# Optimization experiments

Hardware: AMD Instinct MI355X
Metric: run time of the kernel (lower is better)

The kernel has to match this reference:

```python
import jax, jax.numpy as jnp
import numpy as np

BIT = 8      # shared-exponent mantissa bits (bf_conf.*_bit)
GSZ = 36     # block size (bf_conf.*_sz)


def bfp_quantize(x, bit=BIT, sz=GSZ):
    """Block floating point: groups of `sz` consecutive elements share one
    exponent e = floor(log2(max|x|)); each element keeps `bit` mantissa bits."""
    shape = x.shape
    flat = x.reshape(-1)
    n = flat.shape[0]
    pad = (-n) % sz
    flat = jnp.pad(flat, (0, pad))
    g = flat.reshape(-1, sz)                                   # [G, sz]
    maxabs = jnp.max(jnp.abs(g), axis=1, keepdims=True)
    e = jnp.floor(jnp.log2(jnp.where(maxabs > 0, maxabs, 1.0)))
    scale = jnp.exp2(e - (bit - 1))                            # lsb of shared-exp format
    q = jnp.round(g / scale) * scale
    q = jnp.where(maxabs > 0, q, 0.0)
    return q.reshape(-1)[:n].reshape(shape)


def setup_inputs() -> dict:
    key = jax.random.key(0)
    k1, k2, k3 = jax.random.split(key, 3)
    B, Cin, Cout, H, W, K = 16, 32, 32, 224, 224, 3
    x = jax.random.normal(k1, (B, Cin, H, W), dtype=jnp.float32)
    fan_in = Cin * K * K
    bound = 1.0 / np.sqrt(fan_in)
    weight = jax.random.uniform(k2, (Cout, Cin, K, K), jnp.float32, -bound, bound)
    bias = jax.random.uniform(k3, (Cout,), jnp.float32, -bound, bound)
    return {"x": x, "weight": weight, "bias": bias}


def reference(x, weight, bias):
    xq = bfp_quantize(x)          # f_i
    wq = bfp_quantize(weight)     # f_w
    out = jax.lax.conv_general_dilated(
        xq, wq,
        window_strides=(1, 1),
        padding=((1, 1), (1, 1)),
        rhs_dilation=(1, 1),
        feature_group_count=1,
        dimension_numbers=("NCHW", "OIHW", "NCHW"),
    )
    out = out + bias[None, :, None, None]
    out = bfp_quantize(out)       # f_o
    return out
```

## Files before the change

### kernel.cpp

```cpp
#include <hip/hip_runtime.h>
#include <hip/hip_bf16.h>

#define GSZ 36
static const int NX  = 16 * 32 * 224 * 224;
static const int NX4 = NX / 4;
static const int NW  = 32 * 32 * 3 * 3;
static const int GXN = (NX + GSZ - 1) / GSZ;
static const int HWp = 224 * 224;

typedef short bf16x8 __attribute__((ext_vector_type(8)));
typedef float f32x4  __attribute__((ext_vector_type(4)));

__device__ __forceinline__ unsigned div36(unsigned n) {
    return (unsigned)(((unsigned long long)n * 954437177ull) >> 35);
}
__device__ __forceinline__ float scale_from_max(float m) {
    int e = (int)((__float_as_uint(m) >> 23) & 0xffu) - 127;
    return __uint_as_float((unsigned)(e + 120) << 23);
}
__device__ __forceinline__ float inv_from_scale(float s) {
    return __uint_as_float(0x7F000000u - __float_as_uint(s));
}
__device__ __forceinline__ unsigned short f2bf(float f) {
    return (unsigned short)(__float_as_uint(f) >> 16);
}

__global__ void k_quant_wt(const float* __restrict__ w, unsigned short* __restrict__ wt) {
    int g = threadIdx.x;
    int base = g * GSZ;
    float v[GSZ];
    const float4* p = reinterpret_cast<const float4*>(w + base);
    #pragma unroll
    for (int i = 0; i < 9; ++i) {
        float4 t = p[i];
        v[4*i+0] = t.x; v[4*i+1] = t.y; v[4*i+2] = t.z; v[4*i+3] = t.w;
    }
    float m = 0.0f;
    #pragma unroll
    for (int i = 0; i < GSZ; ++i) m = fmaxf(m, fabsf(v[i]));
    if (m > 0.0f) {
        float s = scale_from_max(m), inv = inv_from_scale(s);
        #pragma unroll
        for (int i = 0; i < GSZ; ++i) v[i] = rintf(v[i] * inv) * s;
    }
    #pragma unroll
    for (int i = 0; i < GSZ; ++i) {
        int f = base + i;
        int co = f / 288, rem = f - co * 288;
        int ci = rem / 9, s = rem - ci * 9;
        wt[s * 1024 + co * 32 + ci] = f2bf(v[i]);
    }
}

#define TSTR 452
__global__ __launch_bounds__(256, 4) void k_quant_x_fused(const float* __restrict__ x,
                                                          unsigned short* __restrict__ xt) {
    __shared__ unsigned short tile[32 * TSTR];
    __shared__ float scl[32 * 14];
    __shared__ int rem36s[32], offs[32];

    int t = threadIdx.x;
    int b = blockIdx.y, hp = blockIdx.x;
    int F0 = (b * 32) * HWp + hp * 448;

    if (t < 32) {
        int F = F0 + t * HWp;
        int r = F - 36 * (int)div36((unsigned)F);
        rem36s[t] = r;
        offs[t] = (F - r) & 3;
    }
    for (int i = t; i < 448; i += 256) ((unsigned*)scl)[i] = 0u;
    __syncthreads();

    for (int j = 0; j < 16; ++j) {
        int idx = t + 256 * j;
        int ci = idx >> 7, c4 = idx & 127;
        int off = offs[ci];
        int base4 = F0 + ci * HWp - rem36s[ci] - off;
        int f4 = (base4 >> 2) + c4;
        float4 v = make_float4(0.f, 0.f, 0.f, 0.f);
        if ((unsigned)f4 < (unsigned)NX4)
            v = reinterpret_cast<const float4*>(x)[f4];
        int rel0 = 4 * c4 - off;
        int r0c = rel0 > 0 ? rel0 : 0;
        int gia = (int)div36((unsigned)r0c);
        int bnd = 36 * gia + 36;
        float av[4] = {fabsf(v.x), fabsf(v.y), fabsf(v.z), fabsf(v.w)};
        float ma = 0.f, mb = 0.f;
        #pragma unroll
        for (int k = 0; k < 4; ++k) {
            int rel = rel0 + k;
            float a = ((unsigned)rel < 504u) ? av[k] : 0.f;
            if (rel < bnd) ma = fmaxf(ma, a); else mb = fmaxf(mb, a);
        }
        if (ma > 0.f) atomicMax((unsigned*)&scl[ci * 14 + gia], __float_as_uint(ma));
        if (mb > 0.f) atomicMax((unsigned*)&scl[ci * 14 + gia + 1], __float_as_uint(mb));
    }
    __syncthreads();
    for (int i = t; i < 448; i += 256)
        scl[i] = scale_from_max(__uint_as_float(((unsigned*)scl)[i]));
    __syncthreads();

    for (int j = 0; j < 14; ++j) {
        int eidx = t + 256 * j;
        int ci = ((eidx >> 4) * 293) >> 11;
        int c4 = eidx - ci * 112;
        float4 v = reinterpret_cast<const float4*>(x)[((F0 + ci * HWp) >> 2) + c4];
        int rbase = rem36s[ci] + 4 * c4;
        int gi0 = (int)div36((unsigned)rbase);
        int rr = rbase - 36 * gi0;
        float vv[4] = {v.x, v.y, v.z, v.w};
        unsigned short qb[4];
        #pragma unroll
        for (int k = 0; k < 4; ++k) {
            int gi = gi0 + ((rr + k) >= 36 ? 1 : 0);
            float s = scl[ci * 14 + gi];
            qb[k] = f2bf(rintf(vv[k] * inv_from_scale(s)) * s);
        }
        uint2 o;
        o.x = (unsigned)qb[0] | ((unsigned)qb[1] << 16);
        o.y = (unsigned)qb[2] | ((unsigned)qb[3] << 16);
        *reinterpret_cast<uint2*>(&tile[ci * TSTR + 4 * c4]) = o;
    }
    __syncthreads();

    unsigned short* ob = xt + ((size_t)b * HWp + hp * 448) * 32;
    for (int j = 0; j < 7; ++j) {
        int qd = t + 256 * j;
        int px = qd >> 2;
        int c0 = (qd & 3) * 8;
        unsigned uu[4];
        #pragma unroll
        for (int p = 0; p < 4; ++p) {
            unsigned short lo = tile[(c0 + 2 * p) * TSTR + px];
            unsigned short hi = tile[(c0 + 2 * p + 1) * TSTR + px];
            uu[p] = (unsigned)lo | ((unsigned)hi << 16);
        }
        *reinterpret_cast<uint4*>(ob + (size_t)px * 32 + c0) =
            make_uint4(uu[0], uu[1], uu[2], uu[3]);
    }
}

#define PXS 40
__global__ __launch_bounds__(256, 2) void k_conv_mfma(const unsigned short* __restrict__ xt,
                                                      const unsigned short* __restrict__ wt,
                                                      const float* __restrict__ bias,
                                                      float* __restrict__ out) {
    __shared__ __align__(16) unsigned short xs[18 * 34 * PXS];

    int tid  = threadIdx.x;
    int lane = tid & 63;
    int wid  = tid >> 6;
    int b  = blockIdx.z;
    int h0 = blockIdx.y * 16;
    int w0 = blockIdx.x * 32;

    const unsigned short* xb = xt + (size_t)b * HWp * 32;
    #pragma unroll
    for (int k = 0; k < 10; ++k) {
        int q = tid + k * 256;
        if (q < 2448) {
            int r = q / 136;
            int rem = q - r * 136;
            int p = rem >> 2, ch = rem & 3;
            int gh = h0 + r - 1, gw = w0 + p - 1;
            uint4 val = make_uint4(0u, 0u, 0u, 0u);
            if ((unsigned)gh < 224u && (unsigned)gw < 224u)
                val = *reinterpret_cast<const uint4*>(xb + ((size_t)(gh * 224 + gw)) * 32 + ch * 8);
            *reinterpret_cast<uint4*>(&xs[(r * 34 + p) * PXS + ch * 8]) = val;
        }
    }

    bf16x8 Wf[9][2];
    #pragma unroll
    for (int s = 0; s < 9; ++s)
        #pragma unroll
        for (int hf = 0; hf < 2; ++hf)
            Wf[s][hf] = *reinterpret_cast<const bf16x8*>(
                wt + s * 1024 + (hf * 16 + (lane & 15)) * 32 + (lane >> 4) * 8);

    int m4 = (lane >> 4) << 2;
    f32x4 acc[8][2];
    {
        f32x4 b0, b1;
        #pragma unroll
        for (int r = 0; r < 4; ++r) {
            b0[r] = bias[m4 + r];
            b1[r] = bias[16 + m4 + r];
        }
        #pragma unroll
        for (int g = 0; g < 8; ++g) { acc[g][0] = b0; acc[g][1] = b1; }
    }

    __syncthreads();

    int row4 = wid << 2;
    int kchunk = (lane >> 4) << 3;
    #pragma unroll
    for (int s = 0; s < 9; ++s) {
        int kh = s / 3, kw = s - kh * 3;
        #pragma unroll
        for (int g = 0; g < 8; ++g) {
            int row = row4 + (g >> 1);
            int col = ((g & 1) << 4) + (lane & 15);
            bf16x8 X = *reinterpret_cast<const bf16x8*>(
                &xs[((row + kh) * 34 + col + kw) * PXS + kchunk]);
            acc[g][0] = __builtin_amdgcn_mfma_f32_16x16x32_bf16(Wf[s][0], X, acc[g][0], 0, 0, 0);
            acc[g][1] = __builtin_amdgcn_mfma_f32_16x16x32_bf16(Wf[s][1], X, acc[g][1], 0, 0, 0);
        }
    }

    int pxl = lane & 15;
    #pragma unroll
    for (int g = 0; g < 8; ++g) {
        int h = h0 + row4 + (g >> 1);
        int wl = w0 + ((g & 1) << 4) + pxl;
        size_t base = (size_t)(b * 32) * HWp + h * 224 + wl;
        #pragma unroll
        for (int hf = 0; hf < 2; ++hf)
            #pragma unroll
            for (int r = 0; r < 4; ++r)
                out[base + (size_t)((hf << 4) + m4 + r) * HWp] = acc[g][hf][r];
    }
}

__global__ __launch_bounds__(256, 4) void k_quant_out(float* __restrict__ buf) {
    __shared__ float lds[4 * 2304];
    int t = threadIdx.x, lane = t & 63, wid = t >> 6;
    int gbase = (blockIdx.x * 4 + wid) * 64;
    int f4base = gbase * 9;

    #pragma unroll
    for (int i = 0; i < 9; ++i) {
        int f4 = f4base + i * 64 + lane;
        float4 v = make_float4(0.f, 0.f, 0.f, 0.f);
        if ((unsigned)f4 < (unsigned)NX4) v = reinterpret_cast<const float4*>(buf)[f4];
        *reinterpret_cast<float4*>(&lds[wid * 2304 + (i * 64 + lane) * 4]) = v;
    }
    __syncthreads();

    if (gbase + lane < GXN) {
        float* p = &lds[wid * 2304 + lane * 36];
        f32x4 vv[9];
        #pragma unroll
        for (int i = 0; i < 9; ++i) vv[i] = *reinterpret_cast<f32x4*>(p + 4 * i);
        float m = 0.f;
        #pragma unroll
        for (int i = 0; i < 9; ++i)
            #pragma unroll
            for (int k = 0; k < 4; ++k) m = fmaxf(m, fabsf(vv[i][k]));
        if (m > 0.f) {
            float s = scale_from_max(m), inv = inv_from_scale(s);
            #pragma unroll
            for (int i = 0; i < 9; ++i) {
                #pragma unroll
                for (int k = 0; k < 4; ++k) vv[i][k] = rintf(vv[i][k] * inv) * s;
                *reinterpret_cast<f32x4*>(p + 4 * i) = vv[i];
            }
        }
    }
    __syncthreads();

    #pragma unroll
    for (int i = 0; i < 9; ++i) {
        int f4 = f4base + i * 64 + lane;
        if ((unsigned)f4 < (unsigned)NX4)
            reinterpret_cast<float4*>(buf)[f4] =
                *reinterpret_cast<float4*>(&lds[wid * 2304 + (i * 64 + lane) * 4]);
    }
}

extern "C" void kernel_launch(void* const* d_in, const int* in_sizes, int n_in,
                              void* d_out, int out_size, void* d_ws, size_t ws_size,
                              hipStream_t stream) {
    (void)in_sizes; (void)n_in; (void)out_size; (void)ws_size;
    const float* x    = (const float*)d_in[0];
    const float* w    = (const float*)d_in[1];
    const float* bias = (const float*)d_in[2];
    float* out        = (float*)d_out;

    unsigned short* xt = (unsigned short*)d_ws;
    unsigned short* wt = xt + NX;

    k_quant_wt<<<1, 256, 0, stream>>>(w, wt);
    k_quant_x_fused<<<dim3(112, 16), 256, 0, stream>>>(x, xt);
    k_conv_mfma<<<dim3(7, 14, 16), 256, 0, stream>>>(xt, wt, bias, out);
    k_quant_out<<<2788, 256, 0, stream>>>(out);
}
```

Before: 262.6 us.

## Fuse output BFP quantization into conv epilogue with boundary-group fixup kernel

The conv kernel now has each block compute two full output rows for all 32 channels. It stages the results as bf16 in LDS, derives shared exponents for every 36-element group that lies wholly inside the block, and writes already-quantized fp32 output. A small fixup kernel then re-quantizes the groups that straddle block boundaries. This removes the separate full read-modify-write pass over the output tensor. In exchange the epilogue needs extra LDS staging, barriers and per-element index and division logic. The 512-thread tiling also changes occupancy and the MFMA work per wave.

```diff
diff --git a/kernel.cpp b/kernel.cpp
--- a/kernel.cpp
+++ b/kernel.cpp
@@ -7,6 +7,7 @@
 static const int NW  = 32 * 32 * 3 * 3;
 static const int GXN = (NX + GSZ - 1) / GSZ;
 static const int HWp = 224 * 224;
+static const int NBOUND = NX / 448;
 
 typedef short bf16x8 __attribute__((ext_vector_type(8)));
 typedef float f32x4  __attribute__((ext_vector_type(4)));
@@ -23,6 +24,9 @@
 }
 __device__ __forceinline__ unsigned short f2bf(float f) {
     return (unsigned short)(__float_as_uint(f) >> 16);
+}
+__device__ __forceinline__ float bf2f(unsigned short u) {
+    return __uint_as_float(((unsigned)u) << 16);
 }
 
 __global__ void k_quant_wt(const float* __restrict__ w, unsigned short* __restrict__ wt) {
@@ -141,132 +145,141 @@
     }
 }
 
-#define PXS 40
-__global__ __launch_bounds__(256, 2) void k_conv_mfma(const unsigned short* __restrict__ xt,
-                                                      const unsigned short* __restrict__ wt,
-                                                      const float* __restrict__ bias,
-                                                      float* __restrict__ out) {
-    __shared__ __align__(16) unsigned short xs[18 * 34 * PXS];
+__global__ __launch_bounds__(512, 4) void k_conv_fused(const unsigned short* __restrict__ xt,
+                                                       const unsigned short* __restrict__ wt,
+                                                       const float* __restrict__ bias,
+                                                       float* __restrict__ out) {
+    __shared__ __align__(16) unsigned short smem[4 * 226 * 40];
 
     int tid  = threadIdx.x;
     int lane = tid & 63;
     int wid  = tid >> 6;
-    int b  = blockIdx.z;
-    int h0 = blockIdx.y * 16;
-    int w0 = blockIdx.x * 32;
+    int j = blockIdx.x;
+    int b = blockIdx.y;
+    int h0 = j * 2;
 
     const unsigned short* xb = xt + (size_t)b * HWp * 32;
     #pragma unroll
-    for (int k = 0; k < 10; ++k) {
-        int q = tid + k * 256;
-        if (q < 2448) {
-            int r = q / 136;
-            int rem = q - r * 136;
-            int p = rem >> 2, ch = rem & 3;
-            int gh = h0 + r - 1, gw = w0 + p - 1;
+    for (int it = 0; it < 8; ++it) {
+        int q = tid + it * 512;
+        if (q < 3616) {
+            int r = q / 904, rem = q - r * 904;
+            int px = rem >> 2, c = rem & 3;
+            int gh = h0 - 1 + r, gw = px - 1;
             uint4 val = make_uint4(0u, 0u, 0u, 0u);
             if ((unsigned)gh < 224u && (unsigned)gw < 224u)
-                val = *reinterpret_cast<const uint4*>(xb + ((size_t)(gh * 224 + gw)) * 32 + ch * 8);
-            *reinterpret_cast<uint4*>(&xs[(r * 34 + p) * PXS + ch * 8]) = val;
-        }
-    }
-
-    bf16x8 Wf[9][2];
+                val = *reinterpret_cast<const uint4*>(xb + ((size_t)(gh * 224 + gw)) * 32 + c * 8);
+            *reinterpret_cast<uint4*>(&smem[(r * 226 + px) * 40 + c * 8]) = val;
+        }
+    }
+
+    int row = wid >> 2, cohalf = (wid >> 1) & 1, phalf = wid & 1;
+    int m = lane & 15, kg = lane >> 4;
+    int m4 = kg << 2;
+
+    bf16x8 Wf[9];
     #pragma unroll
     for (int s = 0; s < 9; ++s)
-        #pragma unroll
-        for (int hf = 0; hf < 2; ++hf)
-            Wf[s][hf] = *reinterpret_cast<const bf16x8*>(
-                wt + s * 1024 + (hf * 16 + (lane & 15)) * 32 + (lane >> 4) * 8);
-
-    int m4 = (lane >> 4) << 2;
-    f32x4 acc[8][2];
-    {
-        f32x4 b0, b1;
-        #pragma unroll
-        for (int r = 0; r < 4; ++r) {
-            b0[r] = bias[m4 + r];
-            b1[r] = bias[16 + m4 + r];
-        }
-        #pragma unroll
-        for (int g = 0; g < 8; ++g) { acc[g][0] = b0; acc[g][1] = b1; }
-    }
-
-    __syncthreads();
-
-    int row4 = wid << 2;
-    int kchunk = (lane >> 4) << 3;
+        Wf[s] = *reinterpret_cast<const bf16x8*>(
+            wt + s * 1024 + (cohalf * 16 + m) * 32 + kg * 8);
+
+    f32x4 binit;
+    #pragma unroll
+    for (int r4 = 0; r4 < 4; ++r4) binit[r4] = bias[cohalf * 16 + m4 + r4];
+    f32x4 acc[7];
+    #pragma unroll
+    for (int g = 0; g < 7; ++g) acc[g] = binit;
+
+    __syncthreads();
+
     #pragma unroll
     for (int s = 0; s < 9; ++s) {
         int kh = s / 3, kw = s - kh * 3;
-        #pragma unroll
-        for (int g = 0; g < 8; ++g) {
-            int row = row4 + (g >> 1);
-            int col = ((g & 1) << 4) + (lane & 15);
-            bf16x8 X = *reinterpret_cast<const bf16x8*>(
-                &xs[((row + kh) * 34 + col + kw) * PXS + kchunk]);
-            acc[g][0] = __builtin_amdgcn_mfma_f32_16x16x32_bf16(Wf[s][0], X, acc[g][0], 0, 0, 0);
-            acc[g][1] = __builtin_amdgcn_mfma_f32_16x16x32_bf16(Wf[s][1], X, acc[g][1], 0, 0, 0);
-        }
-    }
-
-    int pxl = lane & 15;
-    #pragma unroll
-    for (int g = 0; g < 8; ++g) {
-        int h = h0 + row4 + (g >> 1);
-        int wl = w0 + ((g & 1) << 4) + pxl;
-        size_t base = (size_t)(b * 32) * HWp + h * 224 + wl;
-        #pragma unroll
-        for (int hf = 0; hf < 2; ++hf)
+        int rbase = (row + kh) * 226;
+        #pragma unroll
+        for (int g = 0; g < 7; ++g) {
+            int px = phalf * 112 + g * 16 + m + kw;
+            bf16x8 X = *reinterpret_cast<const bf16x8*>(&smem[(rbase + px) * 40 + kg * 8]);
+            acc[g] = __builtin_amdgcn_mfma_f32_16x16x32_bf16(Wf[s], X, acc[g], 0, 0, 0);
+        }
+    }
+
+    __syncthreads();
+
+    unsigned short* obuf = smem;
+    float* scl = reinterpret_cast<float*>(smem + 14336);
+
+    #pragma unroll
+    for (int g = 0; g < 7; ++g) {
+        int rp = row * 224 + phalf * 112 + g * 16 + m;
+        #pragma unroll
+        for (int r4 = 0; r4 < 4; ++r4) {
+            int co = cohalf * 16 + m4 + r4;
+            obuf[co * 448 + rp] = f2bf(acc[g][r4]);
+        }
+    }
+    __syncthreads();
+
+    if (tid < 384) {
+        int co = tid / 12, tt = tid - 12 * (tid / 12);
+        int M = 112 * (b * 32 + co) + j;
+        int s36 = (16 * M) % 36;
+        int head = (36 - s36) % 36;
+        int ninter = (448 - head) / 36;
+        if (tt < ninter) {
+            int base = co * 448 + head + 36 * tt;
+            float mx = 0.f;
             #pragma unroll
-            for (int r = 0; r < 4; ++r)
-                out[base + (size_t)((hf << 4) + m4 + r) * HWp] = acc[g][hf][r];
-    }
-}
-
-__global__ __launch_bounds__(256, 4) void k_quant_out(float* __restrict__ buf) {
-    __shared__ float lds[4 * 2304];
-    int t = threadIdx.x, lane = t & 63, wid = t >> 6;
-    int gbase = (blockIdx.x * 4 + wid) * 64;
-    int f4base = gbase * 9;
-
-    #pragma unroll
-    for (int i = 0; i < 9; ++i) {
-        int f4 = f4base + i * 64 + lane;
-        float4 v = make_float4(0.f, 0.f, 0.f, 0.f);
-        if ((unsigned)f4 < (unsigned)NX4) v = reinterpret_cast<const float4*>(buf)[f4];
-        *reinterpret_cast<float4*>(&lds[wid * 2304 + (i * 64 + lane) * 4]) = v;
-    }
-    __syncthreads();
-
-    if (gbase + lane < GXN) {
-        float* p = &lds[wid * 2304 + lane * 36];
-        f32x4 vv[9];
-        #pragma unroll
-        for (int i = 0; i < 9; ++i) vv[i] = *reinterpret_cast<f32x4*>(p + 4 * i);
-        float m = 0.f;
-        #pragma unroll
-        for (int i = 0; i < 9; ++i)
-            #pragma unroll
-            for (int k = 0; k < 4; ++k) m = fmaxf(m, fabsf(vv[i][k]));
-        if (m > 0.f) {
-            float s = scale_from_max(m), inv = inv_from_scale(s);
-            #pragma unroll
-            for (int i = 0; i < 9; ++i) {
-                #pragma unroll
-                for (int k = 0; k < 4; ++k) vv[i][k] = rintf(vv[i][k] * inv) * s;
-                *reinterpret_cast<f32x4*>(p + 4 * i) = vv[i];
+            for (int k = 0; k < 36; ++k) mx = fmaxf(mx, fabsf(bf2f(obuf[base + k])));
+            scl[co * 12 + tt] = (mx > 0.f) ? scale_from_max(mx) : 0.f;
+        }
+    }
+    __syncthreads();
+
+    int head4[4], tail4[4], co4[4];
+    #pragma unroll
+    for (int r4 = 0; r4 < 4; ++r4) {
+        int co = cohalf * 16 + m4 + r4;
+        co4[r4] = co;
+        int M = 112 * (b * 32 + co) + j;
+        int s36 = (16 * M) % 36;
+        int head = (36 - s36) % 36;
+        head4[r4] = head;
+        tail4[r4] = head + 36 * ((448 - head) / 36);
+    }
+    #pragma unroll
+    for (int g = 0; g < 7; ++g) {
+        int wl = phalf * 112 + g * 16 + m;
+        int rp = row * 224 + wl;
+        #pragma unroll
+        for (int r4 = 0; r4 < 4; ++r4) {
+            float v = acc[g][r4];
+            if (rp >= head4[r4] && rp < tail4[r4]) {
+                int t36 = (rp - head4[r4]) / 36;
+                float s = scl[co4[r4] * 12 + t36];
+                if (s != 0.f) v = rintf(v * inv_from_scale(s)) * s;
             }
-        }
-    }
-    __syncthreads();
-
-    #pragma unroll
-    for (int i = 0; i < 9; ++i) {
-        int f4 = f4base + i * 64 + lane;
-        if ((unsigned)f4 < (unsigned)NX4)
-            reinterpret_cast<float4*>(buf)[f4] =
-                *reinterpret_cast<float4*>(&lds[wid * 2304 + (i * 64 + lane) * 4]);
+            out[((size_t)(b * 32 + co4[r4]) * 224 + (h0 + row)) * 224 + wl] = v;
+        }
+    }
+}
+
+__global__ __launch_bounds__(256) void k_fixup(float* __restrict__ out) {
+    int gw = (int)((blockIdx.x * 256 + threadIdx.x) >> 6);
+    int lane = threadIdx.x & 63;
+    int mIdx = gw + 1;
+    if (mIdx >= NBOUND) return;
+    if (mIdx % 9 == 0) return;
+    int f = 448 * mIdx;
+    int base = 36 * (int)div36((unsigned)f);
+    float v = 0.f;
+    if (lane < 36) v = out[base + lane];
+    float a = fabsf(v);
+    #pragma unroll
+    for (int d = 1; d < 64; d <<= 1) a = fmaxf(a, __shfl_xor(a, d));
+    if (lane < 36 && a > 0.f) {
+        float s = scale_from_max(a);
+        out[base + lane] = rintf(v * inv_from_scale(s)) * s;
     }
 }
 
@@ -284,6 +297,6 @@
 
     k_quant_wt<<<1, 256, 0, stream>>>(w, wt);
     k_quant_x_fused<<<dim3(112, 16), 256, 0, stream>>>(x, xt);
-    k_conv_mfma<<<dim3(7, 14, 16), 256, 0, stream>>>(xt, wt, bias, out);
-    k_quant_out<<<2788, 256, 0, stream>>>(out);
-}
+    k_conv_fused<<<dim3(112, 16), 512, 0, stream>>>(xt, wt, bias, out);
+    k_fixup<<<(NBOUND - 1 + 3) / 4, 256, 0, stream>>>(out);
+}
```

New measurement: 265.0 us. Within noise of the previous version (+0.9%).
